# Performance work log

Measured on AMD Instinct MI355X. Metric: run time of the kernel, lower is better.

## Reference

```python
import jax, jax.numpy as jnp
import numpy as np
from jax import lax

B, C, H, W = 8, 256, 128, 128
O = 256
KH, KW = 1, 3
PH, PW = 0, 1
K = KH * KW


def setup_inputs() -> dict:
    key = jax.random.key(0)
    k1, k2, k3, k4 = jax.random.split(key, 4)
    x = jax.random.normal(k1, (B, C, H, W), jnp.float32)
    # offset-predicting conv (small init so sample points stay near the grid)
    offset_w = jax.random.normal(k2, (2 * K, C, KH, KW), jnp.float32) * 0.01
    offset_b = jax.random.normal(k3, (2 * K,), jnp.float32) * 0.01
    # deformable conv weight, no bias (bias=False in the module)
    deform_w = jax.random.normal(k4, (O, C, KH, KW), jnp.float32) * (1.0 / np.sqrt(C * K))
    return {"x": x, "offset_w": offset_w, "offset_b": offset_b, "deform_w": deform_w}


def _gather_corner(x_flat, yi, xi, valid_dtype):
    # x_flat: [B, C, H*W]; yi, xi: int32 [B, K, Ho, Wo]
    valid = (yi >= 0) & (yi < H) & (xi >= 0) & (xi < W)
    yc = jnp.clip(yi, 0, H - 1)
    xc = jnp.clip(xi, 0, W - 1)
    idx = yc * W + xc  # [B, K, Ho, Wo]
    # per-batch fancy gather -> [B, C, K, Ho, Wo]
    g = jax.vmap(lambda f, i: f[:, i])(x_flat, idx)
    return g * valid[:, None].astype(valid_dtype)


def _deform_conv(x, offset, deform_w):
    # torchvision-style deform_conv2d with zero padding, groups=1, dg=1
    Ho, Wo = offset.shape[2], offset.shape[3]
    off = offset.reshape(B, K, 2, Ho, Wo)
    off_y, off_x = off[:, :, 0], off[:, :, 1]  # [B, K, Ho, Wo]

    k = jnp.arange(K)
    base_y = (-PH + (k // KW)).astype(x.dtype)[None, :, None, None]
    base_x = (-PW + (k % KW)).astype(x.dtype)[None, :, None, None]
    grid_y = jnp.arange(Ho, dtype=x.dtype)[None, None, :, None]
    grid_x = jnp.arange(Wo, dtype=x.dtype)[None, None, None, :]

    py = grid_y + base_y + off_y  # fractional sample rows [B,K,Ho,Wo]
    px = grid_x + base_x + off_x  # fractional sample cols

    y0f = jnp.floor(py)
    x0f = jnp.floor(px)
    wy = (py - y0f)[:, None]  # [B,1,K,Ho,Wo]
    wx = (px - x0f)[:, None]
    y0 = y0f.astype(jnp.int32)
    x0 = x0f.astype(jnp.int32)
    y1 = y0 + 1
    x1 = x0 + 1

    x_flat = x.reshape(B, C, H * W)
    v00 = _gather_corner(x_flat, y0, x0, x.dtype)
    v01 = _gather_corner(x_flat, y0, x1, x.dtype)
    v10 = _gather_corner(x_flat, y1, x0, x.dtype)
    v11 = _gather_corner(x_flat, y1, x1, x.dtype)

    sampled = (v00 * (1 - wy) * (1 - wx) + v01 * (1 - wy) * wx
               + v10 * wy * (1 - wx) + v11 * wy * wx)  # [B,C,K,Ho,Wo]

    return jnp.einsum('bckhw,ock->bohw', sampled, deform_w.reshape(O, C, K))


def reference(x, offset_w, offset_b, deform_w):
    # offset conv (stride 1, padding (0,1))
    offset = lax.conv_general_dilated(x, offset_w, window_strides=(1, 1),
                                      padding=[(PH, PH), (PW, PW)])
    offset = offset + offset_b[None, :, None, None]
    # in-place zeroing from the original forward
    offset = offset.at[:, 1].set(0.0).at[:, 4].set(0.0)
    return _deform_conv(x, offset, deform_w)
```

## Files before the change

kernel.cpp:

```cpp
#include <hip/hip_runtime.h>
#include <hip/hip_bf16.h>
#include <hip/hip_fp16.h>

#define Bn 8
#define Cn 256
#define Hn 128
#define Wn 128
#define On 256
#define HWn (Hn*Wn)
#define Pn  HWn
#define Rpad 896
#define W2ROW 768
#define QC  ((size_t)Pn * Cn)

typedef __attribute__((ext_vector_type(8))) short bf16x8;
typedef __attribute__((ext_vector_type(4))) float f32x4;

__device__ __forceinline__ void gload_lds16(const void* g, void* l) {
  __builtin_amdgcn_global_load_lds(
      (__attribute__((address_space(1))) void*)g,
      (__attribute__((address_space(3))) void*)l, 16, 0, 0);
}

__device__ __forceinline__ unsigned short f2bf(float f) {
  unsigned int u = __float_as_uint(f);
  unsigned int r = (u + 0x7fffu + ((u >> 16) & 1u)) >> 16;
  return (unsigned short)r;
}
__device__ __forceinline__ float bf2f(unsigned short u) {
  return __uint_as_float(((unsigned int)u) << 16);
}
__device__ __forceinline__ float h2f(unsigned int u16) {
  return __half2float(__ushort_as_half((unsigned short)u16));
}
__device__ __forceinline__ void bacc(uint4 v, float w, float* f) {
  f[0] += w * __uint_as_float(v.x << 16);
  f[1] += w * __uint_as_float(v.x & 0xffff0000u);
  f[2] += w * __uint_as_float(v.y << 16);
  f[3] += w * __uint_as_float(v.y & 0xffff0000u);
  f[4] += w * __uint_as_float(v.z << 16);
  f[5] += w * __uint_as_float(v.z & 0xffff0000u);
  f[6] += w * __uint_as_float(v.w << 16);
  f[7] += w * __uint_as_float(v.w & 0xffff0000u);
}

__global__ __launch_bounds__(256) void k_wprep(
    const float* __restrict__ dw, const float* __restrict__ ow,
    unsigned short* __restrict__ W2, unsigned short* __restrict__ Wbig) {
  int r = blockIdx.x;
  int c = threadIdx.x;
  float v = 0.f;
  if (r < 768) {
    int k = r >> 8, o = r & 255;
    v = dw[((size_t)o * Cn + c) * 3 + k];
    W2[(size_t)o * W2ROW + k * 256 + c] = f2bf(v);
  } else if (r < 786) {
    int rr = r - 768;
    int oc = rr / 3, kw = rr - 3 * oc;
    v = ow[((size_t)oc * Cn + c) * 3 + kw];
  }
  Wbig[(size_t)r * Cn + c] = f2bf(v);
}

__global__ __launch_bounds__(256) void k_transpose(
    const float* __restrict__ x, unsigned short* __restrict__ xbT) {
  int b = blockIdx.z;
  int q0 = blockIdx.x * 64, c0 = blockIdx.y * 64;
  __shared__ unsigned short t[64][66];
  int tid = threadIdx.x;
  int qi = tid & 63, cg = tid >> 6;
  const float* xb = x + (size_t)b * Cn * HWn;
  #pragma unroll
  for (int i = 0; i < 16; ++i) {
    int cl = i * 4 + cg;
    t[cl][qi] = f2bf(xb[(size_t)(c0 + cl) * HWn + q0 + qi]);
  }
  __syncthreads();
  unsigned short* dst = xbT + (size_t)b * QC;
  int c2 = (tid & 31) * 2, qg = tid >> 5;
  #pragma unroll
  for (int j = 0; j < 8; ++j) {
    int ql = j * 8 + qg;
    unsigned int u = (unsigned int)t[c2][ql] | ((unsigned int)t[c2 + 1][ql] << 16);
    *(unsigned int*)(dst + (size_t)(q0 + ql) * Cn + c0 + c2) = u;
  }
}

__global__ __launch_bounds__(256) void k_goff(
    const unsigned short* __restrict__ xbT,
    const unsigned short* __restrict__ Wbig,
    unsigned short* __restrict__ Goff) {
  int q0 = blockIdx.y * 128;
  const unsigned short* xb = xbT + (size_t)blockIdx.z * QC;
  unsigned short* Gz = Goff + (size_t)blockIdx.z * Pn * 32;
  __shared__ unsigned short Qs[128 * 64];
  __shared__ unsigned short Ws[128 * 64];
  int tid = threadIdx.x;
  int lane = tid & 63, wid = tid >> 6;
  int wr = wid >> 1, wc = wid & 1;
  f32x4 acc[4][4];
  #pragma unroll
  for (int m = 0; m < 4; ++m)
    #pragma unroll
    for (int n = 0; n < 4; ++n) acc[m][n] = (f32x4){0.f, 0.f, 0.f, 0.f};

  for (int kt = 0; kt < 4; ++kt) {
    int ck0 = kt * 64;
    __syncthreads();
    #pragma unroll
    for (int i = 0; i < 4; ++i) {
      int fo = wid * 1024 + i * 4096 + lane * 16;
      int row = fo >> 7;
      int slot = (fo >> 4) & 7;
      int ss = slot ^ (row & 7);
      gload_lds16(xb   + (size_t)(q0 + row) * Cn + ck0 + ss * 8, (char*)Qs + fo);
      gload_lds16(Wbig + (size_t)(768 + row) * Cn + ck0 + ss * 8, (char*)Ws + fo);
    }
    __syncthreads();
    #pragma unroll
    for (int s = 0; s < 2; ++s) {
      bf16x8 af[4], bfr[4];
      #pragma unroll
      for (int m = 0; m < 4; ++m) {
        int row = wr * 64 + m * 16 + (lane & 15);
        int slot = (s * 4 + (lane >> 4)) ^ (row & 7);
        af[m] = *(const bf16x8*)((const char*)Qs + row * 128 + slot * 16);
      }
      #pragma unroll
      for (int n = 0; n < 4; ++n) {
        int row = wc * 64 + n * 16 + (lane & 15);
        int slot = (s * 4 + (lane >> 4)) ^ (row & 7);
        bfr[n] = *(const bf16x8*)((const char*)Ws + row * 128 + slot * 16);
      }
      #pragma unroll
      for (int m = 0; m < 4; ++m)
        #pragma unroll
        for (int n = 0; n < 4; ++n)
          acc[m][n] = __builtin_amdgcn_mfma_f32_16x16x32_bf16(af[m], bfr[n], acc[m][n], 0, 0, 0);
    }
  }
  if (wc == 0) {
    #pragma unroll
    for (int m = 0; m < 4; ++m)
      #pragma unroll
      for (int n = 0; n < 2; ++n)
        #pragma unroll
        for (int rr = 0; rr < 4; ++rr) {
          int q = q0 + wr * 64 + m * 16 + (lane >> 4) * 4 + rr;
          int j = n * 16 + (lane & 15);
          if (j < 18) Gz[(size_t)q * 32 + j] = f2bf(acc[m][n][rr]);
        }
  }
}

__global__ __launch_bounds__(512) void k_fgemm(
    const unsigned short* __restrict__ xbT,
    const unsigned short* __restrict__ W2,
    const unsigned short* __restrict__ Goff,
    const float* __restrict__ obias,
    float* __restrict__ out) {
  int pt = blockIdx.x, z = blockIdx.y;
  int ho = (pt & 7) * 16 + (pt >> 3);
  const unsigned short* xz = xbT + (size_t)z * QC;
  const unsigned short* Gf = Goff + (size_t)z * Pn * 32;

  __shared__ unsigned short Qs[256 * 64];
  __shared__ unsigned short Ss[128 * 64];
  __shared__ unsigned int Sqb[128][3];
  __shared__ unsigned int Swh[128][3][2];

  int tid = threadIdx.x;
  if (tid < 384) {
    int k = tid >> 7;
    int wo = tid & 127;
    float offy = 0.f, offx = 0.f;
    int ocy = 2 * k, ocx = 2 * k + 1;
    if (ocy != 4) {
      float s = obias[ocy];
      #pragma unroll
      for (int kw = 0; kw < 3; ++kw) {
        int col = wo + kw - 1;
        if (col >= 0 && col < Wn)
          s += bf2f(Gf[(size_t)(ho * Wn + col) * 32 + ocy * 3 + kw]);
      }
      offy = s;
    }
    if (ocx != 1) {
      float s = obias[ocx];
      #pragma unroll
      for (int kw = 0; kw < 3; ++kw) {
        int col = wo + kw - 1;
        if (col >= 0 && col < Wn)
          s += bf2f(Gf[(size_t)(ho * Wn + col) * 32 + ocx * 3 + kw]);
      }
      offx = s;
    }
    float py = (float)ho + offy;
    float px = (float)(wo + k - 1) + offx;
    float y0f = floorf(py), x0f = floorf(px);
    float wy = py - y0f, wx = px - x0f;
    int y0 = (int)y0f, x0 = (int)x0f;
    int y1 = y0 + 1, x1 = x0 + 1;
    bool vy0 = (y0 >= 0) && (y0 < Hn), vy1 = (y1 >= 0) && (y1 < Hn);
    bool vx0 = (x0 >= 0) && (x0 < Wn), vx1 = (x1 >= 0) && (x1 < Wn);
    int yc0 = min(max(y0, 0), Hn - 1), yc1 = min(max(y1, 0), Hn - 1);
    int xc0 = min(max(x0, 0), Wn - 1), xc1 = min(max(x1, 0), Wn - 1);
    float w00 = (vy0 && vx0) ? (1.f - wy) * (1.f - wx) : 0.f;
    float w01 = (vy0 && vx1) ? (1.f - wy) * wx : 0.f;
    float w10 = (vy1 && vx0) ? wy * (1.f - wx) : 0.f;
    float w11 = (vy1 && vx1) ? wy * wx : 0.f;
    Sqb[wo][k] = (unsigned)yc0 | ((unsigned)xc0 << 8) | ((unsigned)yc1 << 16) | ((unsigned)xc1 << 24);
    unsigned short h00 = __half_as_ushort(__float2half_rn(w00));
    unsigned short h01 = __half_as_ushort(__float2half_rn(w01));
    unsigned short h10 = __half_as_ushort(__float2half_rn(w10));
    unsigned short h11 = __half_as_ushort(__float2half_rn(w11));
    Swh[wo][k][0] = (unsigned)h00 | ((unsigned)h01 << 16);
    Swh[wo][k][1] = (unsigned)h10 | ((unsigned)h11 << 16);
  }

  int lane = tid & 63, wid = tid >> 6;
  int lg = lane >> 4;
  int wr = wid >> 1, wc = wid & 1;
  int oct = tid & 7, pg = tid >> 3;
  f32x4 acc[4][4];
  #pragma unroll
  for (int m = 0; m < 4; ++m)
    #pragma unroll
    for (int n = 0; n < 4; ++n) acc[m][n] = (f32x4){0.f, 0.f, 0.f, 0.f};

  __syncthreads();

  const char* xzb = (const char*)xz;
  int octo = oct * 16;

  for (int kt = 0; kt < 12; ++kt) {
    int k = kt >> 2;
    int c0 = (kt & 3) << 6;
    __syncthreads();
    #pragma unroll
    for (int i = 0; i < 4; ++i) {
      int t = tid + i * 512;
      int fo = t << 4;
      int row = fo >> 7;
      int slot = (fo >> 4) & 7;
      int ss = slot ^ (row & 7);
      gload_lds16(W2 + (size_t)row * W2ROW + k * 256 + c0 + ss * 8, (char*)Qs + fo);
    }
    const char* bse = xzb + c0 * 2 + octo;
    #pragma unroll
    for (int hh = 0; hh < 2; ++hh) {
      int pl = pg + 64 * hh;
      unsigned qp  = Sqb[pl][k];
      unsigned wlo = Swh[pl][k][0], whi = Swh[pl][k][1];
      int y0o = (int)(qp & 255u) << 16;
      int x0o = (int)((qp >> 8) & 255u) << 9;
      int y1o = (int)((qp >> 16) & 255u) << 16;
      int x1o = (int)(qp >> 24) << 9;
      uint4 v0 = *(const uint4*)(bse + y0o + x0o);
      uint4 v1 = *(const uint4*)(bse + y0o + x1o);
      uint4 v2 = *(const uint4*)(bse + y1o + x0o);
      uint4 v3 = *(const uint4*)(bse + y1o + x1o);
      float f[8] = {0.f, 0.f, 0.f, 0.f, 0.f, 0.f, 0.f, 0.f};
      bacc(v0, h2f(wlo & 0xffffu), f); bacc(v1, h2f(wlo >> 16), f);
      bacc(v2, h2f(whi & 0xffffu), f); bacc(v3, h2f(whi >> 16), f);
      uint4 r;
      r.x = (unsigned)f2bf(f[0]) | ((unsigned)f2bf(f[1]) << 16);
      r.y = (unsigned)f2bf(f[2]) | ((unsigned)f2bf(f[3]) << 16);
      r.z = (unsigned)f2bf(f[4]) | ((unsigned)f2bf(f[5]) << 16);
      r.w = (unsigned)f2bf(f[6]) | ((unsigned)f2bf(f[7]) << 16);
      *(uint4*)((char*)Ss + pl * 128 + ((oct ^ (pl & 7)) << 4)) = r;
    }
    __syncthreads();
    #pragma unroll
    for (int s = 0; s < 2; ++s) {
      bf16x8 af[4], bfr[4];
      #pragma unroll
      for (int m = 0; m < 4; ++m) {
        int row = wr * 64 + m * 16 + (lane & 15);
        int slot = (s * 4 + lg) ^ (row & 7);
        af[m] = *(const bf16x8*)((const char*)Qs + row * 128 + slot * 16);
      }
      #pragma unroll
      for (int n = 0; n < 4; ++n) {
        int row = wc * 64 + n * 16 + (lane & 15);
        int slot = (s * 4 + lg) ^ (row & 7);
        bfr[n] = *(const bf16x8*)((const char*)Ss + row * 128 + slot * 16);
      }
      #pragma unroll
      for (int m = 0; m < 4; ++m)
        #pragma unroll
        for (int n = 0; n < 4; ++n)
          acc[m][n] = __builtin_amdgcn_mfma_f32_16x16x32_bf16(af[m], bfr[n], acc[m][n], 0, 0, 0);
    }
  }

  float* ob_ = out + (size_t)z * On * Pn + (size_t)ho * Wn;
  #pragma unroll
  for (int m = 0; m < 4; ++m)
    #pragma unroll
    for (int n = 0; n < 4; ++n)
      #pragma unroll
      for (int rr = 0; rr < 4; ++rr) {
        int o = wr * 64 + m * 16 + lg * 4 + rr;
        int pc = wc * 64 + n * 16 + (lane & 15);
        ob_[(size_t)o * Pn + pc] = acc[m][n][rr];
      }
}

extern "C" void kernel_launch(void* const* d_in, const int* in_sizes, int n_in,
                              void* d_out, int out_size, void* d_ws, size_t ws_size,
                              hipStream_t stream) {
  const float* x  = (const float*)d_in[0];
  const float* ow = (const float*)d_in[1];
  const float* ob = (const float*)d_in[2];
  const float* dw = (const float*)d_in[3];
  float* out = (float*)d_out;

  char* ws = (char*)d_ws;
  size_t w2_bytes   = (size_t)On * W2ROW * 2;
  size_t wbig_bytes = (size_t)Rpad * Cn * 2;
  size_t xbT_bytes  = QC * 2;
  size_t w2_al   = (w2_bytes + 255) & ~(size_t)255;
  size_t wbig_al = (wbig_bytes + 255) & ~(size_t)255;

  unsigned short* W2   = (unsigned short*)ws;
  unsigned short* Wbig = (unsigned short*)(ws + w2_al);
  unsigned short* xbT  = (unsigned short*)(ws + w2_al + wbig_al);
  unsigned short* Goff = (unsigned short*)(ws + w2_al + wbig_al + (size_t)Bn * xbT_bytes);
  (void)ws_size;

  k_wprep<<<Rpad, 256, 0, stream>>>(dw, ow, W2, Wbig);
  k_transpose<<<dim3(256, 4, Bn), 256, 0, stream>>>(x, xbT);
  k_goff<<<dim3(1, 128, Bn), 256, 0, stream>>>(xbT, Wbig, Goff);
  k_fgemm<<<dim3(128, Bn), 512, 0, stream>>>(xbT, W2, Goff, ob, out);
}
```

Baseline: 180.3 us.

## Fuse transpose and offset-conv projection into a single kernel

Merges the fp32-to-bf16 transpose kernel and the MFMA-based offset projection GEMM into one kernel. While loading x it accumulates the 18 offset channel dot products in fp32 registers, then reduces them across channel groups through shared memory. This removes one launch and the re-read of the transposed bf16 tensor, and drops the padded weight staging. In exchange the projection now runs on scalar FMAs instead of matrix cores, each block reloads the offset weights into LDS, and LDS use and sync count per block grow.

New measurement: 206.0 us. 1.14x slower.

```diff
diff --git a/kernel.cpp b/kernel.cpp
--- a/kernel.cpp
+++ b/kernel.cpp
@@ -9,7 +9,6 @@
 #define On 256
 #define HWn (Hn*Wn)
 #define Pn  HWn
-#define Rpad 896
 #define W2ROW 768
 #define QC  ((size_t)Pn * Cn)
 
@@ -45,111 +44,87 @@
 }
 
 __global__ __launch_bounds__(256) void k_wprep(
-    const float* __restrict__ dw, const float* __restrict__ ow,
-    unsigned short* __restrict__ W2, unsigned short* __restrict__ Wbig) {
+    const float* __restrict__ dw, unsigned short* __restrict__ W2) {
   int r = blockIdx.x;
   int c = threadIdx.x;
-  float v = 0.f;
-  if (r < 768) {
-    int k = r >> 8, o = r & 255;
-    v = dw[((size_t)o * Cn + c) * 3 + k];
-    W2[(size_t)o * W2ROW + k * 256 + c] = f2bf(v);
-  } else if (r < 786) {
-    int rr = r - 768;
-    int oc = rr / 3, kw = rr - 3 * oc;
-    v = ow[((size_t)oc * Cn + c) * 3 + kw];
-  }
-  Wbig[(size_t)r * Cn + c] = f2bf(v);
-}
-
-__global__ __launch_bounds__(256) void k_transpose(
-    const float* __restrict__ x, unsigned short* __restrict__ xbT) {
-  int b = blockIdx.z;
-  int q0 = blockIdx.x * 64, c0 = blockIdx.y * 64;
-  __shared__ unsigned short t[64][66];
+  int k = r >> 8, o = r & 255;
+  W2[(size_t)o * W2ROW + k * 256 + c] = f2bf(dw[((size_t)o * Cn + c) * 3 + k]);
+}
+
+__global__ __launch_bounds__(512) void k_tgoff(
+    const float* __restrict__ x, const float* __restrict__ ow,
+    unsigned short* __restrict__ xbT, unsigned short* __restrict__ Goff) {
+  int b = blockIdx.y;
+  int q0 = blockIdx.x * 64;
+  __shared__ unsigned short t[256][66];
+  __shared__ float wbuf[5120];
   int tid = threadIdx.x;
+  for (int i = tid; i < 4608; i += 512) {
+    int oc = i / 768; int rem = i - oc * 768; int c = rem / 3; int kw = rem - c * 3;
+    wbuf[c * 20 + oc * 3 + kw] = ow[i];
+  }
+  __syncthreads();
+
   int qi = tid & 63, cg = tid >> 6;
-  const float* xb = x + (size_t)b * Cn * HWn;
+  const float* xb = x + (size_t)b * Cn * HWn + q0 + qi;
+  float acc[18];
   #pragma unroll
-  for (int i = 0; i < 16; ++i) {
-    int cl = i * 4 + cg;
-    t[cl][qi] = f2bf(xb[(size_t)(c0 + cl) * HWn + q0 + qi]);
-  }
-  __syncthreads();
-  unsigned short* dst = xbT + (size_t)b * QC;
-  int c2 = (tid & 31) * 2, qg = tid >> 5;
+  for (int j = 0; j < 18; ++j) acc[j] = 0.f;
+  for (int i = 0; i < 32; ++i) {
+    int cl = i * 8 + cg;
+    float v = xb[(size_t)cl * HWn];
+    t[cl][qi] = f2bf(v);
+    const float* wr_ = &wbuf[cl * 20];
+    #pragma unroll
+    for (int j = 0; j < 18; ++j) acc[j] += v * wr_[j];
+  }
+  __syncthreads();
+
+  unsigned short* dst = xbT + (size_t)b * QC + (size_t)q0 * Cn;
+  int c2 = (tid & 127) * 2, qg = tid >> 7;
   #pragma unroll
-  for (int j = 0; j < 8; ++j) {
-    int ql = j * 8 + qg;
-    unsigned int u = (unsigned int)t[c2][ql] | ((unsigned int)t[c2 + 1][ql] << 16);
-    *(unsigned int*)(dst + (size_t)(q0 + ql) * Cn + c0 + c2) = u;
-  }
-}
-
-__global__ __launch_bounds__(256) void k_goff(
-    const unsigned short* __restrict__ xbT,
-    const unsigned short* __restrict__ Wbig,
-    unsigned short* __restrict__ Goff) {
-  int q0 = blockIdx.y * 128;
-  const unsigned short* xb = xbT + (size_t)blockIdx.z * QC;
-  unsigned short* Gz = Goff + (size_t)blockIdx.z * Pn * 32;
-  __shared__ unsigned short Qs[128 * 64];
-  __shared__ unsigned short Ws[128 * 64];
-  int tid = threadIdx.x;
-  int lane = tid & 63, wid = tid >> 6;
-  int wr = wid >> 1, wc = wid & 1;
-  f32x4 acc[4][4];
-  #pragma unroll
-  for (int m = 0; m < 4; ++m)
-    #pragma unroll
-    for (int n = 0; n < 4; ++n) acc[m][n] = (f32x4){0.f, 0.f, 0.f, 0.f};
-
-  for (int kt = 0; kt < 4; ++kt) {
-    int ck0 = kt * 64;
-    __syncthreads();
-    #pragma unroll
-    for (int i = 0; i < 4; ++i) {
-      int fo = wid * 1024 + i * 4096 + lane * 16;
-      int row = fo >> 7;
-      int slot = (fo >> 4) & 7;
-      int ss = slot ^ (row & 7);
-      gload_lds16(xb   + (size_t)(q0 + row) * Cn + ck0 + ss * 8, (char*)Qs + fo);
-      gload_lds16(Wbig + (size_t)(768 + row) * Cn + ck0 + ss * 8, (char*)Ws + fo);
-    }
-    __syncthreads();
-    #pragma unroll
-    for (int s = 0; s < 2; ++s) {
-      bf16x8 af[4], bfr[4];
-      #pragma unroll
-      for (int m = 0; m < 4; ++m) {
-        int row = wr * 64 + m * 16 + (lane & 15);
-        int slot = (s * 4 + (lane >> 4)) ^ (row & 7);
-        af[m] = *(const bf16x8*)((const char*)Qs + row * 128 + slot * 16);
-      }
-      #pragma unroll
-      for (int n = 0; n < 4; ++n) {
-        int row = wc * 64 + n * 16 + (lane & 15);
-        int slot = (s * 4 + (lane >> 4)) ^ (row & 7);
-        bfr[n] = *(const bf16x8*)((const char*)Ws + row * 128 + slot * 16);
-      }
-      #pragma unroll
-      for (int m = 0; m < 4; ++m)
-        #pragma unroll
-        for (int n = 0; n < 4; ++n)
-          acc[m][n] = __builtin_amdgcn_mfma_f32_16x16x32_bf16(af[m], bfr[n], acc[m][n], 0, 0, 0);
-    }
-  }
-  if (wc == 0) {
-    #pragma unroll
-    for (int m = 0; m < 4; ++m)
-      #pragma unroll
-      for (int n = 0; n < 2; ++n)
-        #pragma unroll
-        for (int rr = 0; rr < 4; ++rr) {
-          int q = q0 + wr * 64 + m * 16 + (lane >> 4) * 4 + rr;
-          int j = n * 16 + (lane & 15);
-          if (j < 18) Gz[(size_t)q * 32 + j] = f2bf(acc[m][n][rr]);
-        }
+  for (int j = 0; j < 16; ++j) {
+    int ql = j * 4 + qg;
+    unsigned u = (unsigned)t[c2][ql] | ((unsigned)t[c2 + 1][ql] << 16);
+    *(unsigned*)(dst + (size_t)ql * Cn + c2) = u;
+  }
+
+  float* red = wbuf;
+  if (cg >= 4) {
+    float* rp = &red[((cg - 4) * 64 + qi) * 18];
+    #pragma unroll
+    for (int j = 0; j < 18; ++j) rp[j] = acc[j];
+  }
+  __syncthreads();
+  if (cg < 4) {
+    const float* rp = &red[(cg * 64 + qi) * 18];
+    #pragma unroll
+    for (int j = 0; j < 18; ++j) acc[j] += rp[j];
+  }
+  __syncthreads();
+  if (cg >= 2 && cg < 4) {
+    float* rp = &red[((cg - 2) * 64 + qi) * 18];
+    #pragma unroll
+    for (int j = 0; j < 18; ++j) rp[j] = acc[j];
+  }
+  __syncthreads();
+  if (cg < 2) {
+    const float* rp = &red[(cg * 64 + qi) * 18];
+    #pragma unroll
+    for (int j = 0; j < 18; ++j) acc[j] += rp[j];
+  }
+  __syncthreads();
+  if (cg == 1) {
+    float* rp = &red[qi * 18];
+    #pragma unroll
+    for (int j = 0; j < 18; ++j) rp[j] = acc[j];
+  }
+  __syncthreads();
+  if (cg == 0) {
+    const float* rp = &red[qi * 18];
+    unsigned short* Gz = Goff + (size_t)b * Pn * 32 + (size_t)(q0 + qi) * 32;
+    #pragma unroll
+    for (int j = 0; j < 18; ++j) Gz[j] = f2bf(acc[j] + rp[j]);
   }
 }
 
@@ -318,19 +293,15 @@
 
   char* ws = (char*)d_ws;
   size_t w2_bytes   = (size_t)On * W2ROW * 2;
-  size_t wbig_bytes = (size_t)Rpad * Cn * 2;
   size_t xbT_bytes  = QC * 2;
   size_t w2_al   = (w2_bytes + 255) & ~(size_t)255;
-  size_t wbig_al = (wbig_bytes + 255) & ~(size_t)255;
 
   unsigned short* W2   = (unsigned short*)ws;
-  unsigned short* Wbig = (unsigned short*)(ws + w2_al);
-  unsigned short* xbT  = (unsigned short*)(ws + w2_al + wbig_al);
-  unsigned short* Goff = (unsigned short*)(ws + w2_al + wbig_al + (size_t)Bn * xbT_bytes);
+  unsigned short* xbT  = (unsigned short*)(ws + w2_al);
+  unsigned short* Goff = (unsigned short*)(ws + w2_al + (size_t)Bn * xbT_bytes);
   (void)ws_size;
 
-  k_wprep<<<Rpad, 256, 0, stream>>>(dw, ow, W2, Wbig);
-  k_transpose<<<dim3(256, 4, Bn), 256, 0, stream>>>(x, xbT);
-  k_goff<<<dim3(1, 128, Bn), 256, 0, stream>>>(xbT, Wbig, Goff);
+  k_wprep<<<768, 256, 0, stream>>>(dw, W2);
+  k_tgoff<<<dim3(256, Bn), 512, 0, stream>>>(x, ow, xbT, Goff);
   k_fgemm<<<dim3(128, Bn), 512, 0, stream>>>(xbT, W2, Goff, ob, out);
 }
```
